# Optimization experiments

Measured on AMD Instinct MI355X. Metric: run time of the kernel, lower is better.

Reference implementation:

```python
import jax, jax.numpy as jnp
import numpy as np

NUM_HEADS = 8
EPS = 1e-12  # torch F.normalize eps

def _conv(x, w, padding, groups=1):
    return jax.lax.conv_general_dilated(
        x, w, window_strides=(1, 1), padding=padding,
        dimension_numbers=('NCHW', 'OIHW', 'NCHW'),
        feature_group_count=groups)

def setup_inputs() -> dict:
    key = jax.random.key(0)
    ks = jax.random.split(key, 5)
    b, dim, h, w = 8, 192, 128, 128
    kv = jax.random.normal(ks[0], (b, dim, h, w), dtype=jnp.float32)
    q = jax.random.normal(ks[1], (b, dim, h, w), dtype=jnp.float32)
    qkv1_w = jax.random.normal(ks[2], (2 * dim, dim, 1, 1), dtype=jnp.float32) * (1.0 / np.sqrt(dim))
    qkv2_w = jax.random.normal(ks[3], (2 * dim, 1, 3, 3), dtype=jnp.float32) * (1.0 / 3.0)
    proj_w = jax.random.normal(ks[4], (dim, dim, 1, 1), dtype=jnp.float32) * (1.0 / np.sqrt(dim))
    scale = jnp.ones((NUM_HEADS, 1, 1), dtype=jnp.float32)
    return {"kv": kv, "q": q, "qkv1_w": qkv1_w, "qkv2_w": qkv2_w,
            "proj_w": proj_w, "scale": scale}

def reference(kv, q, qkv1_w, qkv2_w, proj_w, scale):
    b, c, h, w = kv.shape
    head = NUM_HEADS
    cd = c // head  # channels per head
    hw = h * w
    # 1x1 conv dim -> 2*dim, then 3x3 depthwise conv (groups = 2*dim)
    kv_f = _conv(kv, qkv1_w, padding='VALID')
    kv_f = _conv(kv_f, qkv2_w, padding=((1, 1), (1, 1)), groups=2 * c)
    k, v = jnp.split(kv_f, 2, axis=1)
    # rearrange to [b, head, c, hw]
    qh = q.reshape(b, head, cd, hw)
    kh = k.reshape(b, head, cd, hw)
    vh = v.reshape(b, head, cd, hw)
    # L2-normalize along spatial dim (torch F.normalize semantics)
    qh = qh / jnp.maximum(jnp.linalg.norm(qh, axis=-1, keepdims=True), EPS)
    kh = kh / jnp.maximum(jnp.linalg.norm(kh, axis=-1, keepdims=True), EPS)
    # channel attention: [b, head, c, c]
    attn = jnp.einsum('bhcn,bhdn->bhcd', qh, kh) * scale  # scale broadcasts [head,1,1]
    attn = jax.nn.softmax(attn, axis=-1)
    out = jnp.einsum('bhcd,bhdn->bhcn', attn, vh)  # [b, head, c, hw]
    out = out.reshape(b, c, h, w)
    out = _conv(out, proj_w, padding='VALID')
    return out
```

## Files before the change

kernel.cpp:

```cpp
#include <hip/hip_runtime.h>
#include <hip/hip_bf16.h>

#define HW 16384
#define DIM 192
#define DIM2 384
#define NB 8
#define HEADS 8
#define CD 24
#define NSPLIT 64

typedef float f32x4 __attribute__((ext_vector_type(4)));
typedef short bf16x8 __attribute__((ext_vector_type(8)));
typedef short s16x4 __attribute__((ext_vector_type(4)));

__device__ __forceinline__ short f2bf(float f) {
    __hip_bfloat16 h = __float2bfloat16(f);
    return *reinterpret_cast<short*>(&h);
}
__device__ __forceinline__ float bf2f(short s) {
    __hip_bfloat16 h = *reinterpret_cast<__hip_bfloat16*>(&s);
    return __bfloat162float(h);
}

__global__ __launch_bounds__(256)
void prep_w1(const float* __restrict__ w1, short* __restrict__ wb1)
{
    int idx = blockIdx.x * 256 + threadIdx.x;
    if (idx >= 9216) return;
    int mi = idx / 384, rem = idx % 384;
    int c = rem >> 6, l = rem & 63;
    int oc = mi * 16 + (l & 15);
    int kb = c * 32 + (l >> 4) * 8;
    const float* src = w1 + (long)oc * DIM + kb;
    float4 v0 = *reinterpret_cast<const float4*>(src);
    float4 v1 = *reinterpret_cast<const float4*>(src + 4);
    bf16x8 o;
    o[0]=f2bf(v0.x); o[1]=f2bf(v0.y); o[2]=f2bf(v0.z); o[3]=f2bf(v0.w);
    o[4]=f2bf(v1.x); o[5]=f2bf(v1.y); o[6]=f2bf(v1.z); o[7]=f2bf(v1.w);
    *reinterpret_cast<bf16x8*>(wb1 + (long)idx * 8) = o;
}

template<int NOCT, bool B_F32, bool PER_BATCH_A, bool OUT_F32>
__global__ __launch_bounds__(256, 2)
void gemm_k192(const short* __restrict__ Ab, const void* __restrict__ Bg,
               void* __restrict__ Cg, long bstrideB, long bstrideC)
{
    __shared__ short lds[128 * 200];
    __shared__ float eps[4][16 * 36];
    const int tid  = threadIdx.x;
    const int lane = tid & 63;
    const int wave = tid >> 6;
    const int pxbase = blockIdx.x * 256;
    const int b    = blockIdx.y;

    const int row  = lane & 15;
    const int kgrp = lane >> 4;
    const short* A0 = Ab + (PER_BATCH_A ? (long)b * NOCT * 3072 : 0);

    bf16x8 aA[6], aB[6];
    auto loadA = [&](bf16x8* dst, int mi) {
#pragma unroll
        for (int c = 0; c < 6; c++)
            dst[c] = *reinterpret_cast<const bf16x8*>(
                &A0[((long)(mi * 6 + c) * 64 + lane) * 8]);
    };

    const int q  = tid & 31;
    const int kl = tid >> 5;
    f32x4 stf[6][4];
    s16x4 sth[6][4];
    auto SLOAD = [&](int px0) {
        if constexpr (B_F32) {
            const float* src = (const float*)Bg + (long)b * bstrideB + px0 + q * 4;
#pragma unroll
            for (int j = 0; j < 6; j++)
#pragma unroll
                for (int e = 0; e < 4; e++)
                    stf[j][e] = __builtin_nontemporal_load(
                        reinterpret_cast<const f32x4*>(src + (long)(32 * j + 4 * kl + e) * HW));
        } else {
            const short* src = (const short*)Bg + (long)b * bstrideB + px0 + q * 4;
#pragma unroll
            for (int j = 0; j < 6; j++)
#pragma unroll
                for (int e = 0; e < 4; e++)
                    sth[j][e] = __builtin_nontemporal_load(
                        reinterpret_cast<const s16x4*>(src + (long)(32 * j + 4 * kl + e) * HW));
        }
    };
    auto SWRITE = [&]() {
        const int goff = (((kl >> 1) ^ (q & 3)) << 3) + (kl & 1) * 4;
#pragma unroll
        for (int j = 0; j < 6; j++) {
#pragma unroll
            for (int i = 0; i < 4; i++) {
                s16x4 t;
                if constexpr (B_F32)
                    t = (s16x4){f2bf(stf[j][0][i]), f2bf(stf[j][1][i]),
                                f2bf(stf[j][2][i]), f2bf(stf[j][3][i])};
                else
                    t = (s16x4){sth[j][0][i], sth[j][1][i], sth[j][2][i], sth[j][3][i]};
                *(s16x4*)&lds[(q * 4 + i) * 200 + 32 * j + goff] = t;
            }
        }
    };

    bf16x8 bv[2][6];
    auto HOIST = [&]() {
        const int bro = wave * 32 + row;
        const int sgr = (row >> 2) & 3;
#pragma unroll
        for (int c = 0; c < 6; c++) {
            bv[0][c] = *(const bf16x8*)&lds[bro * 200 + c * 32 + ((kgrp ^ sgr) << 3)];
            bv[1][c] = *(const bf16x8*)&lds[(bro + 16) * 200 + c * 32 + ((kgrp ^ sgr) << 3)];
        }
    };

    const int oc8  = lane >> 3;
    const int pxq8 = lane & 7;
    float* ep = &eps[wave][0];
    auto computeStore = [&](const bf16x8* a, int mi, int px0) {
        f32x4 acc0 = (f32x4){0.f, 0.f, 0.f, 0.f};
        f32x4 acc1 = (f32x4){0.f, 0.f, 0.f, 0.f};
#pragma unroll
        for (int c = 0; c < 6; c++) {
            acc0 = __builtin_amdgcn_mfma_f32_16x16x32_bf16(a[c], bv[0][c], acc0, 0, 0, 0);
            acc1 = __builtin_amdgcn_mfma_f32_16x16x32_bf16(a[c], bv[1][c], acc1, 0, 0, 0);
        }
#pragma unroll
        for (int r = 0; r < 4; r++) {
            ep[(kgrp * 4 + r) * 36 + row]      = acc0[r];
            ep[(kgrp * 4 + r) * 36 + 16 + row] = acc1[r];
        }
#pragma unroll
        for (int rr = 0; rr < 2; rr++) {
            const int oc16 = oc8 + rr * 8;
            f32x4 vv = *reinterpret_cast<const f32x4*>(&ep[oc16 * 36 + pxq8 * 4]);
            long off = (long)b * bstrideC + (long)(mi * 16 + oc16) * HW
                     + px0 + wave * 32 + pxq8 * 4;
            if constexpr (OUT_F32) {
                __builtin_nontemporal_store(vv, reinterpret_cast<f32x4*>((float*)Cg + off));
            } else {
                *reinterpret_cast<s16x4*>((short*)Cg + off) =
                    (s16x4){f2bf(vv[0]), f2bf(vv[1]), f2bf(vv[2]), f2bf(vv[3])};
            }
        }
    };
    auto COMPUTE = [&](int px0) {
        for (int mi = 0; mi < NOCT; mi += 2) {
            loadA(aB, mi + 1);
            computeStore(aA, mi, px0);
            if (mi + 2 < NOCT) loadA(aA, mi + 2);
            computeStore(aB, mi + 1, px0);
        }
    };

    loadA(aA, 0);
    SLOAD(pxbase);
    SWRITE();
    __syncthreads();
    HOIST();
    __syncthreads();
    SLOAD(pxbase + 128);
    COMPUTE(pxbase);
    loadA(aA, 0);
    SWRITE();
    __syncthreads();
    HOIST();
    COMPUTE(pxbase + 128);
}

__global__ __launch_bounds__(256)
void dwconv_sumsq(const short* __restrict__ in, const float* __restrict__ w2,
                  short* __restrict__ outp, float* __restrict__ kss)
{
    __shared__ float red[4];
    const long bgc = blockIdx.x;
    const int  gc  = (int)(bgc % DIM2);
    const int  b   = (int)(bgc / DIM2);
    const int  tid = threadIdx.x;
    const int  tx  = tid & 15;
    const int  ty  = tid >> 4;
    const int  lane = tid & 63;
    const int  x0 = tx * 8;
    const int  y0 = ty * 8;
    const short* src = in + (bgc << 14);
    short* dst = outp + (bgc << 14);

    float w[9];
#pragma unroll
    for (int i = 0; i < 9; i++) w[i] = w2[gc * 9 + i];

    float r0[10], r1[10], r2[10];
    auto loadRow = [&](float* r, int y) {
        if ((unsigned)y > 127u) {
#pragma unroll
            for (int i = 0; i < 10; i++) r[i] = 0.f;
            return;
        }
        bf16x8 v = *reinterpret_cast<const bf16x8*>(&src[y * 128 + x0]);
#pragma unroll
        for (int i = 0; i < 8; i++) r[i + 1] = bf2f(v[i]);
        float left  = __shfl(r[8], lane - 1);
        float right = __shfl(r[1], lane + 1);
        r[0] = (tx == 0)  ? 0.f : left;
        r[9] = (tx == 15) ? 0.f : right;
    };

    loadRow(r0, y0 - 1);
    loadRow(r1, y0);
    float ssq = 0.f;
#pragma unroll
    for (int k = 0; k < 8; k++) {
        const int yy = y0 + k;
        loadRow(r2, yy + 1);
        bf16x8 o;
#pragma unroll
        for (int j = 0; j < 8; j++) {
            float s = r0[j] * w[0] + r0[j + 1] * w[1] + r0[j + 2] * w[2]
                    + r1[j] * w[3] + r1[j + 1] * w[4] + r1[j + 2] * w[5]
                    + r2[j] * w[6] + r2[j + 1] * w[7] + r2[j + 2] * w[8];
            o[j] = f2bf(s);
            ssq += s * s;
        }
        *reinterpret_cast<bf16x8*>(&dst[yy * 128 + x0]) = o;
#pragma unroll
        for (int i = 0; i < 10; i++) { r0[i] = r1[i]; r1[i] = r2[i]; }
    }

    for (int o = 32; o; o >>= 1) ssq += __shfl_xor(ssq, o);
    if ((tid & 63) == 0) red[tid >> 6] = ssq;
    __syncthreads();
    if (gc < DIM && tid == 0)
        kss[b * DIM + gc] = red[0] + red[1] + red[2] + red[3];
}

__global__ __launch_bounds__(64)
void qk_mfma(const float* __restrict__ q, const short* __restrict__ kvb,
             float* __restrict__ part, float* __restrict__ pssq)
{
    const int split = blockIdx.x;
    const int bh    = blockIdx.y;
    const int b = bh >> 3, h = bh & 7;
    const int lane = threadIdx.x;
    const int row = lane & 15;
    const int kg  = (lane >> 4) * 8;
    const int CHUNK = HW / NSPLIT;

    const int qr1 = min(h * CD + 16 + row, DIM - 1);
    const float* q0 = q + ((long)b * DIM + h * CD + row) * HW + split * CHUNK + kg;
    const float* q1 = q + ((long)b * DIM + qr1) * HW + split * CHUNK + kg;
    const short* k0 = kvb + ((long)b * DIM2 + h * CD + row) * HW + split * CHUNK + kg;
    const short* k1 = k0 + 16L * HW;

    f32x4 acc[2][2];
#pragma unroll
    for (int m = 0; m < 2; m++)
#pragma unroll
        for (int n = 0; n < 2; n++) acc[m][n] = (f32x4){0.f, 0.f, 0.f, 0.f};
    float ssq0 = 0.f, ssq1 = 0.f;

#pragma unroll
    for (int s = 0; s < CHUNK / 32; s++) {
        const int px = s * 32;
        float4 qa = *reinterpret_cast<const float4*>(q0 + px);
        float4 qb = *reinterpret_cast<const float4*>(q0 + px + 4);
        float4 qc = *reinterpret_cast<const float4*>(q1 + px);
        float4 qd = *reinterpret_cast<const float4*>(q1 + px + 4);
        bf16x8 b0 = *reinterpret_cast<const bf16x8*>(k0 + px);
        bf16x8 b1 = *reinterpret_cast<const bf16x8*>(k1 + px);
        ssq0 += qa.x*qa.x + qa.y*qa.y + qa.z*qa.z + qa.w*qa.w
              + qb.x*qb.x + qb.y*qb.y + qb.z*qb.z + qb.w*qb.w;
        ssq1 += qc.x*qc.x + qc.y*qc.y + qc.z*qc.z + qc.w*qc.w
              + qd.x*qd.x + qd.y*qd.y + qd.z*qd.z + qd.w*qd.w;
        bf16x8 a0, a1;
        a0[0]=f2bf(qa.x); a0[1]=f2bf(qa.y); a0[2]=f2bf(qa.z); a0[3]=f2bf(qa.w);
        a0[4]=f2bf(qb.x); a0[5]=f2bf(qb.y); a0[6]=f2bf(qb.z); a0[7]=f2bf(qb.w);
        a1[0]=f2bf(qc.x); a1[1]=f2bf(qc.y); a1[2]=f2bf(qc.z); a1[3]=f2bf(qc.w);
        a1[4]=f2bf(qd.x); a1[5]=f2bf(qd.y); a1[6]=f2bf(qd.z); a1[7]=f2bf(qd.w);
        acc[0][0] = __builtin_amdgcn_mfma_f32_16x16x32_bf16(a0, b0, acc[0][0], 0, 0, 0);
        acc[0][1] = __builtin_amdgcn_mfma_f32_16x16x32_bf16(a0, b1, acc[0][1], 0, 0, 0);
        acc[1][0] = __builtin_amdgcn_mfma_f32_16x16x32_bf16(a1, b0, acc[1][0], 0, 0, 0);
        acc[1][1] = __builtin_amdgcn_mfma_f32_16x16x32_bf16(a1, b1, acc[1][1], 0, 0, 0);
    }

    ssq0 += __shfl_xor(ssq0, 16); ssq0 += __shfl_xor(ssq0, 32);
    ssq1 += __shfl_xor(ssq1, 16); ssq1 += __shfl_xor(ssq1, 32);

    float* pd = part + ((long)split * 64 + bh) * 576;
#pragma unroll
    for (int m = 0; m < 2; m++)
#pragma unroll
        for (int n = 0; n < 2; n++)
#pragma unroll
            for (int r = 0; r < 4; r++) {
                int c = m * 16 + (lane >> 4) * 4 + r;
                int d = n * 16 + row;
                if (c < CD && d < CD) pd[c * CD + d] = acc[m][n][r];
            }
    if (lane < 16) {
        float* ps = pssq + ((long)split * 64 + bh) * 32;
        ps[lane]      = ssq0;
        ps[16 + lane] = ssq1;
    }
}

__global__ __launch_bounds__(256)
void softmax_buildm(const float* __restrict__ part, const float* __restrict__ pssq,
                    const float* __restrict__ kss, const float* __restrict__ scale,
                    const float* __restrict__ pw, short* __restrict__ M)
{
    __shared__ float probL[CD][CD + 1];
    __shared__ float qsL[CD];
    const int bh = blockIdx.x;
    const int b = bh >> 3, h = bh & 7;
    const int t = threadIdx.x;

    if (t < CD) {
        float qs = 0.f;
        for (int s = 0; s < NSPLIT; s++) qs += pssq[((long)s * 64 + bh) * 32 + t];
        qsL[t] = qs;
    }
    __syncthreads();

    const int dd = t & 31;
    const float sc = scale[h];
#pragma unroll
    for (int p = 0; p < 3; p++) {
        const int c = p * 8 + (t >> 5);
        float val = -1e30f;
        if (dd < CD) {
            float raw = 0.f;
            for (int s = 0; s < NSPLIT; s++)
                raw += part[((long)s * 64 + bh) * 576 + c * CD + dd];
            float qn = fmaxf(sqrtf(qsL[c]), 1e-12f);
            float kn = fmaxf(sqrtf(kss[b * DIM + h * CD + dd]), 1e-12f);
            val = raw * sc / (qn * kn);
        }
        float m = val;
        for (int o = 16; o; o >>= 1) m = fmaxf(m, __shfl_xor(m, o, 32));
        float e = (dd < CD) ? expf(val - m) : 0.f;
        float s = e;
        for (int o = 16; o; o >>= 1) s += __shfl_xor(s, o, 32);
        if (dd < CD) probL[c][dd] = e / s;
    }
    __syncthreads();

    for (int w = 0; w < 3; w++) {
        const int fid = w * 256 + t;
        if (fid >= 576) break;
        const int mi   = fid / 48;
        const int r    = fid % 48;
        const int row  = r & 15;
        const int gi   = r >> 4;
        const int gvc0 = h * CD + gi * 8;
        const int cf   = gvc0 >> 5;
        const int kge  = (gvc0 >> 3) & 3;
        const int l    = (kge << 4) | row;
        const int oc   = mi * 16 + row;
        bf16x8 o;
#pragma unroll
        for (int e = 0; e < 8; e++) {
            const int d = gi * 8 + e;
            float s = 0.f;
#pragma unroll
            for (int cc = 0; cc < CD; cc++)
                s += pw[oc * DIM + h * CD + cc] * probL[cc][d];
            o[e] = f2bf(s);
        }
        long idx = (long)b * 4608 + mi * 384 + cf * 64 + l;
        *reinterpret_cast<bf16x8*>(M + idx * 8) = o;
    }
}

extern "C" void kernel_launch(void* const* d_in, const int* in_sizes, int n_in,
                              void* d_out, int out_size, void* d_ws, size_t ws_size,
                              hipStream_t stream)
{
    const float* kv    = (const float*)d_in[0];
    const float* q     = (const float*)d_in[1];
    const float* w1    = (const float*)d_in[2];
    const float* w2    = (const float*)d_in[3];
    const float* pw    = (const float*)d_in[4];
    const float* scale = (const float*)d_in[5];
    float* out = (float*)d_out;

    char* ws = (char*)d_ws;
    long off = 0;
    auto alloc = [&](long bytes) { char* p = ws + off; off += (bytes + 255) & ~255L; return p; };
    short* kvf1 = (short*)alloc((long)NB * DIM2 * HW * 2);
    short* kvb  = (short*)alloc((long)NB * DIM2 * HW * 2);
    short* wb1  = (short*)alloc((long)DIM2 * DIM * 2);
    float* kss  = (float*)alloc((long)NB * DIM * 4);
    float* part = (float*)alloc((long)NSPLIT * 64 * 576 * 4);
    float* pssq = (float*)alloc((long)NSPLIT * 64 * 32 * 4);
    short* M    = (short*)alloc((long)NB * DIM * DIM * 2);

    prep_w1<<<36, 256, 0, stream>>>(w1, wb1);

    gemm_k192<24, true, false, false><<<dim3(64, NB), 256, 0, stream>>>(
        wb1, kv, kvf1, (long)DIM * HW, (long)DIM2 * HW);

    dwconv_sumsq<<<NB * DIM2, 256, 0, stream>>>(kvf1, w2, kvb, kss);

    qk_mfma<<<dim3(NSPLIT, 64), 64, 0, stream>>>(q, kvb, part, pssq);

    softmax_buildm<<<64, 256, 0, stream>>>(part, pssq, kss, scale, pw, M);

    gemm_k192<12, false, true, true><<<dim3(64, NB), 256, 0, stream>>>(
        M, kvb + (long)DIM * HW, out, (long)DIM2 * HW, (long)DIM * HW);
}
```

Before: 179.7 us.

## Process head pairs per block in qk_mfma to eliminate padded tile waste

Each qk_mfma block now handles two adjacent heads (48 channels) as three 16-row tiles and computes only the 7 block-diagonal-relevant 16x16 MFMA tiles, instead of one head with a padded 32x32 tile layout that reloaded rows beyond the head. This removes redundant q/k row loads, since the old code read 32 rows to use 24, and halves the block count. The pssq layout changes to match, and softmax_buildm indexes it accordingly. Fewer, heavier blocks may reduce memory-level parallelism for this bandwidth-bound stage.

Result: no change. 177.6 us (median of 2 runs) (-1.1%).

```diff
diff --git a/kernel.cpp b/kernel.cpp
--- a/kernel.cpp
+++ b/kernel.cpp
@@ -240,68 +240,71 @@
              float* __restrict__ part, float* __restrict__ pssq)
 {
     const int split = blockIdx.x;
-    const int bh    = blockIdx.y;
-    const int b = bh >> 3, h = bh & 7;
+    const int g     = blockIdx.y;
+    const int b = g >> 2, hp = g & 3;
     const int lane = threadIdx.x;
     const int row = lane & 15;
     const int kg  = (lane >> 4) * 8;
     const int CHUNK = HW / NSPLIT;
 
-    const int qr1 = min(h * CD + 16 + row, DIM - 1);
-    const float* q0 = q + ((long)b * DIM + h * CD + row) * HW + split * CHUNK + kg;
-    const float* q1 = q + ((long)b * DIM + qr1) * HW + split * CHUNK + kg;
-    const short* k0 = kvb + ((long)b * DIM2 + h * CD + row) * HW + split * CHUNK + kg;
-    const short* k1 = k0 + 16L * HW;
-
-    f32x4 acc[2][2];
-#pragma unroll
-    for (int m = 0; m < 2; m++)
-#pragma unroll
-        for (int n = 0; n < 2; n++) acc[m][n] = (f32x4){0.f, 0.f, 0.f, 0.f};
-    float ssq0 = 0.f, ssq1 = 0.f;
+    const float* qm[3];
+    const short* km[3];
+#pragma unroll
+    for (int t = 0; t < 3; t++) {
+        qm[t] = q   + ((long)b * DIM  + hp * 48 + t * 16 + row) * HW + split * CHUNK + kg;
+        km[t] = kvb + ((long)b * DIM2 + hp * 48 + t * 16 + row) * HW + split * CHUNK + kg;
+    }
+
+    const int MT[7] = {0,0,1,1,1,2,2};
+    const int NT[7] = {0,1,0,1,2,1,2};
+    f32x4 acc[7];
+#pragma unroll
+    for (int p = 0; p < 7; p++) acc[p] = (f32x4){0.f, 0.f, 0.f, 0.f};
+    float ssq[3] = {0.f, 0.f, 0.f};
 
 #pragma unroll
     for (int s = 0; s < CHUNK / 32; s++) {
         const int px = s * 32;
-        float4 qa = *reinterpret_cast<const float4*>(q0 + px);
-        float4 qb = *reinterpret_cast<const float4*>(q0 + px + 4);
-        float4 qc = *reinterpret_cast<const float4*>(q1 + px);
-        float4 qd = *reinterpret_cast<const float4*>(q1 + px + 4);
-        bf16x8 b0 = *reinterpret_cast<const bf16x8*>(k0 + px);
-        bf16x8 b1 = *reinterpret_cast<const bf16x8*>(k1 + px);
-        ssq0 += qa.x*qa.x + qa.y*qa.y + qa.z*qa.z + qa.w*qa.w
-              + qb.x*qb.x + qb.y*qb.y + qb.z*qb.z + qb.w*qb.w;
-        ssq1 += qc.x*qc.x + qc.y*qc.y + qc.z*qc.z + qc.w*qc.w
-              + qd.x*qd.x + qd.y*qd.y + qd.z*qd.z + qd.w*qd.w;
-        bf16x8 a0, a1;
-        a0[0]=f2bf(qa.x); a0[1]=f2bf(qa.y); a0[2]=f2bf(qa.z); a0[3]=f2bf(qa.w);
-        a0[4]=f2bf(qb.x); a0[5]=f2bf(qb.y); a0[6]=f2bf(qb.z); a0[7]=f2bf(qb.w);
-        a1[0]=f2bf(qc.x); a1[1]=f2bf(qc.y); a1[2]=f2bf(qc.z); a1[3]=f2bf(qc.w);
-        a1[4]=f2bf(qd.x); a1[5]=f2bf(qd.y); a1[6]=f2bf(qd.z); a1[7]=f2bf(qd.w);
-        acc[0][0] = __builtin_amdgcn_mfma_f32_16x16x32_bf16(a0, b0, acc[0][0], 0, 0, 0);
-        acc[0][1] = __builtin_amdgcn_mfma_f32_16x16x32_bf16(a0, b1, acc[0][1], 0, 0, 0);
-        acc[1][0] = __builtin_amdgcn_mfma_f32_16x16x32_bf16(a1, b0, acc[1][0], 0, 0, 0);
-        acc[1][1] = __builtin_amdgcn_mfma_f32_16x16x32_bf16(a1, b1, acc[1][1], 0, 0, 0);
-    }
-
-    ssq0 += __shfl_xor(ssq0, 16); ssq0 += __shfl_xor(ssq0, 32);
-    ssq1 += __shfl_xor(ssq1, 16); ssq1 += __shfl_xor(ssq1, 32);
-
-    float* pd = part + ((long)split * 64 + bh) * 576;
-#pragma unroll
-    for (int m = 0; m < 2; m++)
-#pragma unroll
-        for (int n = 0; n < 2; n++)
-#pragma unroll
-            for (int r = 0; r < 4; r++) {
-                int c = m * 16 + (lane >> 4) * 4 + r;
-                int d = n * 16 + row;
-                if (c < CD && d < CD) pd[c * CD + d] = acc[m][n][r];
+        bf16x8 a[3], bvv[3];
+#pragma unroll
+        for (int t = 0; t < 3; t++) {
+            float4 qa = *reinterpret_cast<const float4*>(qm[t] + px);
+            float4 qb = *reinterpret_cast<const float4*>(qm[t] + px + 4);
+            ssq[t] += qa.x*qa.x + qa.y*qa.y + qa.z*qa.z + qa.w*qa.w
+                    + qb.x*qb.x + qb.y*qb.y + qb.z*qb.z + qb.w*qb.w;
+            a[t][0]=f2bf(qa.x); a[t][1]=f2bf(qa.y); a[t][2]=f2bf(qa.z); a[t][3]=f2bf(qa.w);
+            a[t][4]=f2bf(qb.x); a[t][5]=f2bf(qb.y); a[t][6]=f2bf(qb.z); a[t][7]=f2bf(qb.w);
+            bvv[t] = *reinterpret_cast<const bf16x8*>(km[t] + px);
+        }
+#pragma unroll
+        for (int p = 0; p < 7; p++)
+            acc[p] = __builtin_amdgcn_mfma_f32_16x16x32_bf16(a[MT[p]], bvv[NT[p]], acc[p], 0, 0, 0);
+    }
+
+#pragma unroll
+    for (int t = 0; t < 3; t++) {
+        ssq[t] += __shfl_xor(ssq[t], 16);
+        ssq[t] += __shfl_xor(ssq[t], 32);
+    }
+    if (lane < 16) {
+        float* ps = pssq + ((long)split * 32 + g) * 48;
+#pragma unroll
+        for (int t = 0; t < 3; t++) ps[t * 16 + lane] = ssq[t];
+    }
+
+#pragma unroll
+    for (int p = 0; p < 7; p++) {
+#pragma unroll
+        for (int r = 0; r < 4; r++) {
+            const int c48 = MT[p] * 16 + (lane >> 4) * 4 + r;
+            const int d48 = NT[p] * 16 + row;
+            const int hc = c48 >= CD, hd = d48 >= CD;
+            if (hc == hd) {
+                const int bh = b * 8 + hp * 2 + hc;
+                part[((long)split * 64 + bh) * 576 + (c48 - hc * CD) * CD + (d48 - hd * CD)]
+                    = acc[p][r];
             }
-    if (lane < 16) {
-        float* ps = pssq + ((long)split * 64 + bh) * 32;
-        ps[lane]      = ssq0;
-        ps[16 + lane] = ssq1;
+        }
     }
 }
 
@@ -317,8 +320,9 @@
     const int t = threadIdx.x;
 
     if (t < CD) {
+        const long gidx = (long)(b * 4 + (h >> 1)) * 48 + (h & 1) * CD + t;
         float qs = 0.f;
-        for (int s = 0; s < NSPLIT; s++) qs += pssq[((long)s * 64 + bh) * 32 + t];
+        for (int s = 0; s < NSPLIT; s++) qs += pssq[(long)s * 32 * 48 + gidx];
         qsL[t] = qs;
     }
     __syncthreads();
@@ -393,7 +397,7 @@
     short* wb1  = (short*)alloc((long)DIM2 * DIM * 2);
     float* kss  = (float*)alloc((long)NB * DIM * 4);
     float* part = (float*)alloc((long)NSPLIT * 64 * 576 * 4);
-    float* pssq = (float*)alloc((long)NSPLIT * 64 * 32 * 4);
+    float* pssq = (float*)alloc((long)NSPLIT * 32 * 48 * 4);
     short* M    = (short*)alloc((long)NB * DIM * DIM * 2);
 
     prep_w1<<<36, 256, 0, stream>>>(w1, wb1);
@@ -403,7 +407,7 @@
 
     dwconv_sumsq<<<NB * DIM2, 256, 0, stream>>>(kvf1, w2, kvb, kss);
 
-    qk_mfma<<<dim3(NSPLIT, 64), 64, 0, stream>>>(q, kvb, part, pssq);
+    qk_mfma<<<dim3(NSPLIT, 32), 64, 0, stream>>>(q, kvb, part, pssq);
 
     softmax_buildm<<<64, 256, 0, stream>>>(part, pssq, kss, scale, pw, M);
 
```
